# Kernel tuning notes

Hardware: AMD Instinct MI355X
Metric: run time of the kernel (lower is better)

Reference implementation:

```python
import jax, jax.numpy as jnp
import numpy as np

CHEB_K = 2  # chebyshev polynomial order (support_ks = [I, A] for cheb_k=2)


def _fc(x, w1, b1, w2, b2, w3, b3):
    # FC module: Linear -> sigmoid -> Linear -> sigmoid -> Linear
    h = jax.nn.sigmoid(x @ w1 + b1)
    h = jax.nn.sigmoid(h @ w2 + b2)
    return h @ w3 + b3


def _preprocess(adj):
    # adj: [B,N,N]; add self-loops then row-normalize
    adj = adj + jnp.eye(adj.shape[-1], dtype=adj.dtype)
    return adj / adj.sum(-1, keepdims=True)


def _gcn(x, adjs, ne, wpool, bpool):
    # x: [B,N,C], adjs: list of [B,N,N], ne: [N,E]
    # wpool: [E, 2*CHEB_K, C, O], bpool: [E, O]
    mats = []
    for A in adjs:
        ks = [jnp.broadcast_to(jnp.eye(A.shape[-1], dtype=A.dtype), A.shape), A]
        for _ in range(2, CHEB_K):
            ks.append(2.0 * jnp.matmul(A, ks[-1]) - ks[-2])
        mats.extend(ks)
    # [B,N,K,C] with K = 2*CHEB_K
    x_g = jnp.stack([jnp.einsum('bnm,bmc->bnc', S, x) for S in mats], axis=2)
    weights = jnp.einsum('nd,dkio->nkio', ne, wpool)  # [N,K,C,O]
    bias = ne @ bpool  # [N,O]
    return jnp.einsum('bnki,nkio->bno', x_g, weights) + bias


def _forward(x, state, ne0, ne1, ne2, fc1_w1, fc1_b1, fc1_w2, fc1_b2, fc1_w3, fc1_b3,
             fc2_w1, fc2_b1, fc2_w2, fc2_b2, fc2_w3, fc2_b3, gate_w, gate_b, upd_w, upd_b):
    hid = upd_w.shape[-1]
    ins = jnp.concatenate([x, state], axis=-1)  # [B,N,dim_in+hid]
    f1 = _fc(ins, fc1_w1, fc1_b1, fc1_w2, fc1_b2, fc1_w3, fc1_b3)  # [B,N,TD]
    f2 = _fc(ins, fc2_w1, fc2_b1, fc2_w2, fc2_b2, fc2_w3, fc2_b3)
    nv1 = jnp.tanh(ne0[:, None, :] * f1)  # einsum 'bd,bnd->bnd' == broadcast mul
    nv2 = jnp.tanh(ne1[:, None, :] * f2)
    adj = jnp.einsum('bnd,bmd->bnm', nv1, nv2) - jnp.einsum('bnd,bmd->bnm', nv2, nv1)
    adj1 = _preprocess(jax.nn.relu(adj))
    adj2 = _preprocess(jax.nn.relu(-jnp.swapaxes(adj, -2, -1)))
    z_r = jax.nn.sigmoid(_gcn(ins, [adj1, adj2], ne2, gate_w, gate_b))
    z, r = z_r[..., :hid], z_r[..., hid:]
    cand = jnp.concatenate([x, z * state], axis=-1)
    hc = jnp.tanh(_gcn(cand, [adj1, adj2], ne2, upd_w, upd_b))
    return r * state + (1.0 - r) * hc


def setup_inputs():
    B, N, DIN, DOUT, ED, TD = 32, 1024, 2, 64, 10, 32
    HG, MID = 16, 2  # hyperGNN_dim, middle_dim hardcoded in FC
    CIN = DIN + DOUT
    K2 = 2 * CHEB_K
    ks = jax.random.split(jax.random.key(0), 16)
    rn = lambda i, shape, s=1.0: jax.random.normal(ks[i], shape, dtype=jnp.float32) * s
    return {
        'x': rn(0, (B, N, DIN)),
        'state': rn(1, (B, N, DOUT)),
        'ne0': rn(2, (B, TD)),
        'ne1': rn(3, (B, TD)),
        'ne2': rn(4, (N, ED), 0.1),
        'fc1_w1': rn(5, (CIN, HG), 0.1), 'fc1_b1': jnp.zeros((HG,), jnp.float32),
        'fc1_w2': rn(6, (HG, MID), 0.1), 'fc1_b2': jnp.zeros((MID,), jnp.float32),
        'fc1_w3': rn(7, (MID, TD), 0.1), 'fc1_b3': jnp.zeros((TD,), jnp.float32),
        'fc2_w1': rn(8, (CIN, HG), 0.1), 'fc2_b1': jnp.zeros((HG,), jnp.float32),
        'fc2_w2': rn(9, (HG, MID), 0.1), 'fc2_b2': jnp.zeros((MID,), jnp.float32),
        'fc2_w3': rn(10, (MID, TD), 0.1), 'fc2_b3': jnp.zeros((TD,), jnp.float32),
        'gate_w': rn(11, (ED, K2, CIN, 2 * DOUT), 0.1),
        'gate_b': rn(12, (ED, 2 * DOUT), 0.1),
        'upd_w': rn(13, (ED, K2, CIN, DOUT), 0.1),
        'upd_b': rn(14, (ED, DOUT), 0.1),
    }


def reference(x, state, ne0, ne1, ne2, fc1_w1, fc1_b1, fc1_w2, fc1_b2, fc1_w3, fc1_b3,
              fc2_w1, fc2_b1, fc2_w2, fc2_b2, fc2_w3, fc2_b3, gate_w, gate_b, upd_w, upd_b):
    return _forward(x, state, ne0, ne1, ne2, fc1_w1, fc1_b1, fc1_w2, fc1_b2, fc1_w3, fc1_b3,
                    fc2_w1, fc2_b1, fc2_w2, fc2_b2, fc2_w3, fc2_b3, gate_w, gate_b, upd_w, upd_b)
```

## Files before the change

### kernel.cpp

```cpp
#include <hip/hip_runtime.h>
#include <math.h>

#define BB   32
#define NN   1024
#define DIN  2
#define DOUT 64
#define CIN  66
#define TD   32
#define ED   10
#define OG   128
#define OU   64
#define KP   160
#define XTR  80
#define PS   88

typedef __bf16 bf16x8 __attribute__((ext_vector_type(8)));
typedef float  f32x4  __attribute__((ext_vector_type(4)));
typedef short  s16x8  __attribute__((ext_vector_type(8)));

__device__ __forceinline__ unsigned short f2b(float f) {
    __bf16 h = (__bf16)f;
    return *(unsigned short*)&h;
}

__global__ __launch_bounds__(256) void k_pre(
    const float* __restrict__ x, const float* __restrict__ state,
    const float* __restrict__ ne0, const float* __restrict__ ne1,
    const float* __restrict__ ne2,
    const float* __restrict__ w11, const float* __restrict__ b11,
    const float* __restrict__ w12, const float* __restrict__ b12,
    const float* __restrict__ w13, const float* __restrict__ b13,
    const float* __restrict__ w21, const float* __restrict__ b21,
    const float* __restrict__ w22, const float* __restrict__ b22,
    const float* __restrict__ w23, const float* __restrict__ b23,
    const float* __restrict__ gate_w, const float* __restrict__ gate_b,
    const float* __restrict__ upd_w, const float* __restrict__ upd_b,
    unsigned short* __restrict__ nv1b, unsigned short* __restrict__ nv2b,
    unsigned short* __restrict__ XT0, unsigned short* __restrict__ XT1,
    unsigned short* __restrict__ BcTg, unsigned short* __restrict__ BcTu,
    float* __restrict__ biasG, float* __restrict__ biasU)
{
    __shared__ float sw[2408];
    __shared__ unsigned short st[68*72];
    int blk = blockIdx.x;
    int t = threadIdx.x;

    if (blk < 128) {
        const int oW1 = 0, oB1 = 1056, oW2 = 1072, oB2 = 1104, oW3 = 1108, oB3 = 1172, F2 = 1204;
        for (int i = t; i < 1056; i += 256) { sw[oW1+i] = w11[i]; sw[F2+oW1+i] = w21[i]; }
        if (t < 16) { sw[oB1+t] = b11[t]; sw[F2+oB1+t] = b21[t]; }
        if (t < 32) { sw[oW2+t] = w12[t]; sw[F2+oW2+t] = w22[t]; }
        if (t < 2)  { sw[oB2+t] = b12[t]; sw[F2+oB2+t] = b22[t]; }
        if (t < 64) { sw[oW3+t] = w13[t]; sw[F2+oW3+t] = w23[t]; }
        if (t >= 64 && t < 96) { sw[oB3+t-64] = b13[t-64]; sw[F2+oB3+t-64] = b23[t-64]; }
        __syncthreads();

        int p = blk*256 + t;
        int b = p >> 10;

        float h1a[16], h1b[16];
        #pragma unroll
        for (int j = 0; j < 16; ++j) { h1a[j] = sw[oB1+j]; h1b[j] = sw[F2+oB1+j]; }
        for (int i = 0; i < CIN; ++i) {
            float v = (i < DIN) ? x[(size_t)p*DIN + i] : state[(size_t)p*DOUT + (i-DIN)];
            #pragma unroll
            for (int jq = 0; jq < 4; ++jq) {
                float4 wa = *(const float4*)&sw[oW1 + i*16 + jq*4];
                float4 wb = *(const float4*)&sw[F2 + oW1 + i*16 + jq*4];
                h1a[jq*4+0] += v*wa.x; h1a[jq*4+1] += v*wa.y;
                h1a[jq*4+2] += v*wa.z; h1a[jq*4+3] += v*wa.w;
                h1b[jq*4+0] += v*wb.x; h1b[jq*4+1] += v*wb.y;
                h1b[jq*4+2] += v*wb.z; h1b[jq*4+3] += v*wb.w;
            }
        }
        #pragma unroll
        for (int j = 0; j < 16; ++j) {
            h1a[j] = 1.f/(1.f + __expf(-h1a[j]));
            h1b[j] = 1.f/(1.f + __expf(-h1b[j]));
        }
        float h2a0 = sw[oB2+0], h2a1 = sw[oB2+1];
        float h2b0 = sw[F2+oB2+0], h2b1 = sw[F2+oB2+1];
        #pragma unroll
        for (int i = 0; i < 16; ++i) {
            h2a0 += h1a[i]*sw[oW2 + i*2 + 0];
            h2a1 += h1a[i]*sw[oW2 + i*2 + 1];
            h2b0 += h1b[i]*sw[F2+oW2 + i*2 + 0];
            h2b1 += h1b[i]*sw[F2+oW2 + i*2 + 1];
        }
        h2a0 = 1.f/(1.f + __expf(-h2a0)); h2a1 = 1.f/(1.f + __expf(-h2a1));
        h2b0 = 1.f/(1.f + __expf(-h2b0)); h2b1 = 1.f/(1.f + __expf(-h2b1));

        const float* pn0 = ne0 + b*TD;
        const float* pn1 = ne1 + b*TD;
        #pragma unroll
        for (int jq = 0; jq < 8; ++jq) {
            float4 ba  = *(const float4*)&sw[oB3 + jq*4];
            float4 wa0 = *(const float4*)&sw[oW3 + jq*4];
            float4 wa1 = *(const float4*)&sw[oW3 + 32 + jq*4];
            float4 bb2 = *(const float4*)&sw[F2+oB3 + jq*4];
            float4 wb0 = *(const float4*)&sw[F2+oW3 + jq*4];
            float4 wb1 = *(const float4*)&sw[F2+oW3 + 32 + jq*4];
            float4 n0 = *(const float4*)&pn0[jq*4];
            float4 n1 = *(const float4*)&pn1[jq*4];
            ushort4 u1, u2;
            u1.x = f2b(tanhf(n0.x*(ba.x + h2a0*wa0.x + h2a1*wa1.x)));
            u1.y = f2b(tanhf(n0.y*(ba.y + h2a0*wa0.y + h2a1*wa1.y)));
            u1.z = f2b(tanhf(n0.z*(ba.z + h2a0*wa0.z + h2a1*wa1.z)));
            u1.w = f2b(tanhf(n0.w*(ba.w + h2a0*wa0.w + h2a1*wa1.w)));
            u2.x = f2b(tanhf(n1.x*(bb2.x + h2b0*wb0.x + h2b1*wb1.x)));
            u2.y = f2b(tanhf(n1.y*(bb2.y + h2b0*wb0.y + h2b1*wb1.y)));
            u2.z = f2b(tanhf(n1.z*(bb2.z + h2b0*wb0.z + h2b1*wb1.z)));
            u2.w = f2b(tanhf(n1.w*(bb2.w + h2b0*wb0.w + h2b1*wb1.w)));
            *(ushort4*)&nv1b[(size_t)p*TD + jq*4] = u1;
            *(ushort4*)&nv2b[(size_t)p*TD + jq*4] = u2;
        }
    } else if (blk < 640) {
        int idx = blk - 128;
        int b = idx >> 4, m0 = (idx & 15)*64;
        for (int i = t; i < 1024; i += 256) {
            int m = i >> 4, cq = i & 15;
            size_t base = (size_t)b*NN + m0 + m;
            float4 v = *(const float4*)&state[base*DOUT + cq*4];
            st[(2 + cq*4 + 0)*72 + m] = f2b(v.x);
            st[(2 + cq*4 + 1)*72 + m] = f2b(v.y);
            st[(2 + cq*4 + 2)*72 + m] = f2b(v.z);
            st[(2 + cq*4 + 3)*72 + m] = f2b(v.w);
        }
        if (t < 128) {
            int m = t >> 1, c = t & 1;
            st[c*72 + m] = f2b(x[((size_t)b*NN + m0 + m)*DIN + c]);
        }
        __syncthreads();
        const unsigned int ONE2 = 0x3F803F80u;
        for (int i = t; i < XTR*8; i += 256) {
            int c = i >> 3, ch = i & 7;
            uint4 v;
            if (c < 66)      v = *(const uint4*)&st[c*72 + ch*8];
            else if (c == 66) v = make_uint4(ONE2, ONE2, ONE2, ONE2);
            else              v = make_uint4(0, 0, 0, 0);
            *(uint4*)&XT0[((size_t)b*XTR + c)*NN + m0 + ch*8] = v;
            if (c < 2 || c >= 66)
                *(uint4*)&XT1[((size_t)b*XTR + c)*NN + m0 + ch*8] = v;
        }
    } else if (blk < 1840) {
        int tid = (blk - 640)*256 + t;
        int c = tid / KP, k = tid - c*KP;
        const float* pool; int O, cc; unsigned short* dst;
        if (c < 1280) { pool = gate_w; O = OG; cc = c;        dst = BcTg; }
        else          { pool = upd_w;  O = OU; cc = c - 1280; dst = BcTu; }
        int d = cc / O, o = cc - d*O;
        float v = 0.f;
        if (k < 132) {
            int kp = (k < 66) ? 0 : 1;
            int i  = (k < 66) ? k : k - 66;
            v = pool[(size_t)((d*4 + kp)*CIN + i)*O + o]
              + pool[(size_t)((d*4 + kp + 2)*CIN + i)*O + o];
        }
        dst[(size_t)cc*KP + k] = f2b(v);
    } else {
        int i = (blk - 1840)*256 + t;
        int n = i / 192, j = i - n*192;
        float v = 0.f;
        if (j < 128) {
            #pragma unroll
            for (int d = 0; d < ED; ++d) v += ne2[(size_t)n*ED + d]*gate_b[d*OG + j];
            biasG[(size_t)n*OG + j] = v;
        } else {
            int o = j - 128;
            #pragma unroll
            for (int d = 0; d < ED; ++d) v += ne2[(size_t)n*ED + d]*upd_b[d*OU + o];
            biasU[(size_t)n*OU + o] = v;
        }
    }
}

__global__ __launch_bounds__(512) void k_aapply(
    const unsigned short* __restrict__ nv1b, const unsigned short* __restrict__ nv2b,
    const unsigned short* __restrict__ XTg, unsigned short* __restrict__ A)
{
    __shared__ unsigned short s_nv1r[64*40], s_nv2r[64*40];
    __shared__ unsigned short s_nv1c[64*40], s_nv2c[64*40];
    __shared__ unsigned short s_p[64*PS];
    __shared__ unsigned short s_xt[80*72];
    __shared__ float s_rs[64];

    int t = threadIdx.x;
    int id = blockIdx.x;
    int b = id & 31, rbase = (id >> 5)*64;
    int w = t >> 6, lane = t & 63, lq = lane >> 4, ln = lane & 15;
    int g = w >> 1, sub = w & 1;

    {
        int arr = t >> 8, j = t & 255;
        int node = j >> 2, ch = j & 3;
        const unsigned short* src = (arr ? nv2b : nv1b)
            + ((size_t)b*NN + rbase + node)*TD + ch*8;
        unsigned short* dst = (arr ? s_nv2r : s_nv1r) + node*40 + ch*8;
        *(uint4*)dst = *(const uint4*)src;
    }
    __syncthreads();

    bf16x8 a1 = *(const bf16x8*)&s_nv1r[(16*g + ln)*40 + lq*8];
    s16x8 a2s = *(const s16x8*)&s_nv2r[(16*g + ln)*40 + lq*8];
    const s16x8 sgn = {(short)0x8000,(short)0x8000,(short)0x8000,(short)0x8000,
                       (short)0x8000,(short)0x8000,(short)0x8000,(short)0x8000};
    a2s ^= sgn;
    bf16x8 a2n = (bf16x8)a2s;

    f32x4 acc[3];
    #pragma unroll
    for (int i = 0; i < 3; ++i) acc[i] = (f32x4){0.f,0.f,0.f,0.f};
    const f32x4 zero4 = {0.f,0.f,0.f,0.f};

    for (int mb = 0; mb < NN; mb += 64) {
        __syncthreads();
        {
            int arr = t >> 8, j = t & 255;
            int node = j >> 2, ch = j & 3;
            const unsigned short* src = (arr ? nv2b : nv1b)
                + ((size_t)b*NN + mb + node)*TD + ch*8;
            unsigned short* dst = (arr ? s_nv2c : s_nv1c) + node*40 + ch*8;
            *(uint4*)dst = *(const uint4*)src;
        }
        for (int i = t; i < 640; i += 512) {
            int c = i >> 3, ch = i & 7;
            *(uint4*)&s_xt[c*72 + ch*8] =
                *(const uint4*)&XTg[((size_t)b*XTR + c)*NN + mb + ch*8];
        }
        __syncthreads();

        #pragma unroll
        for (int jj = 0; jj < 2; ++jj) {
            int j0 = (sub*2 + jj)*16;
            bf16x8 b2 = *(const bf16x8*)&s_nv2c[(j0 + ln)*40 + lq*8];
            bf16x8 b1 = *(const bf16x8*)&s_nv1c[(j0 + ln)*40 + lq*8];
            f32x4 s = __builtin_amdgcn_mfma_f32_16x16x32_bf16(a1,  b2, zero4, 0, 0, 0);
            s       = __builtin_amdgcn_mfma_f32_16x16x32_bf16(a2n, b1, s,     0, 0, 0);
            #pragma unroll
            for (int r = 0; r < 4; ++r) {
                float p = fmaxf(s[r], 0.f);
                *(__bf16*)&s_p[(16*g + lq*4 + r)*PS + j0 + ln] = (__bf16)p;
            }
        }
        __syncthreads();

        bf16x8 pa0 = *(const bf16x8*)&s_p[(16*g + ln)*PS +      lq*8];
        bf16x8 pa1 = *(const bf16x8*)&s_p[(16*g + ln)*PS + 32 + lq*8];
        if (sub == 0) {
            #pragma unroll
            for (int k = 0; k < 3; ++k) {
                int n0 = k*16;
                bf16x8 xb0 = *(const bf16x8*)&s_xt[(n0 + ln)*72 +      lq*8];
                bf16x8 xb1 = *(const bf16x8*)&s_xt[(n0 + ln)*72 + 32 + lq*8];
                acc[k] = __builtin_amdgcn_mfma_f32_16x16x32_bf16(pa0, xb0, acc[k], 0, 0, 0);
                acc[k] = __builtin_amdgcn_mfma_f32_16x16x32_bf16(pa1, xb1, acc[k], 0, 0, 0);
            }
        } else {
            #pragma unroll
            for (int k = 0; k < 2; ++k) {
                int n0 = (3 + k)*16;
                bf16x8 xb0 = *(const bf16x8*)&s_xt[(n0 + ln)*72 +      lq*8];
                bf16x8 xb1 = *(const bf16x8*)&s_xt[(n0 + ln)*72 + 32 + lq*8];
                acc[k] = __builtin_amdgcn_mfma_f32_16x16x32_bf16(pa0, xb0, acc[k], 0, 0, 0);
                acc[k] = __builtin_amdgcn_mfma_f32_16x16x32_bf16(pa1, xb1, acc[k], 0, 0, 0);
            }
        }
    }

    if (sub == 1 && ln == 2) {
        #pragma unroll
        for (int r = 0; r < 4; ++r) s_rs[16*g + lq*4 + r] = acc[1][r];
    }
    __syncthreads();
    float rinv[4];
    #pragma unroll
    for (int r = 0; r < 4; ++r) rinv[r] = 1.0f / (1.0f + s_rs[16*g + lq*4 + r]);

    int kmax = sub ? 2 : 3;
    for (int k = 0; k < kmax; ++k) {
        int c = (sub ? (3 + k) : k)*16 + ln;
        if (c < CIN) {
            #pragma unroll
            for (int r = 0; r < 4; ++r) {
                int gr = rbase + 16*g + lq*4 + r;
                size_t rowG = (size_t)b*NN + gr;
                unsigned short xu = XTg[((size_t)b*XTR + c)*NN + gr];
                float xr = (float)(*(const __bf16*)&xu);
                A[rowG*KP + c]      = xu;
                A[rowG*KP + 66 + c] = f2b((acc[k][r] + xr) * rinv[r]);
            }
        }
    }
    for (int i = t; i < 64*28; i += 512) {
        int rr = i / 28, cc = 132 + (i - 28*(i/28));
        A[((size_t)b*NN + rbase + rr)*KP + cc] = 0;
    }
}

template<int O, int MODE>
__global__ __launch_bounds__(256) void k_gemm(
    const unsigned short* __restrict__ A, const unsigned short* __restrict__ BcT,
    const float* __restrict__ ne2, const float* __restrict__ biasP,
    const float* __restrict__ state, unsigned short* __restrict__ XT1,
    float* __restrict__ rbuf, float* __restrict__ out)
{
    __shared__ unsigned short s_b[80*168];

    int t = threadIdx.x;
    int w = t >> 6, lane = t & 63, lq = lane >> 4, ln = lane & 15;
    int o0 = blockIdx.y*16;
    int rowBlock = blockIdx.x*128;
    int rowW = rowBlock + w*32;

    f32x4 acc[2][2][5];
    #pragma unroll
    for (int h = 0; h < 2; ++h)
        #pragma unroll
        for (int f = 0; f < 2; ++f)
            #pragma unroll
            for (int c = 0; c < 5; ++c) acc[h][f][c] = (f32x4){0.f,0.f,0.f,0.f};

    #pragma unroll
    for (int h = 0; h < 2; ++h) {
        if (h) __syncthreads();
        for (int i = t; i < 1600; i += 256) {
            int cc = i / 20, kc = i - cc*20;
            int d = h*5 + (cc >> 4), oo = cc & 15;
            *(uint4*)&s_b[cc*168 + kc*8] =
                *(const uint4*)&BcT[(size_t)(d*O + o0 + oo)*KP + kc*8];
        }
        __syncthreads();

        #pragma unroll
        for (int kc = 0; kc < 5; ++kc) {
            bf16x8 af0 = *(const bf16x8*)&A[(size_t)(rowW      + ln)*KP + kc*32 + lq*8];
            bf16x8 af1 = *(const bf16x8*)&A[(size_t)(rowW + 16 + ln)*KP + kc*32 + lq*8];
            #pragma unroll
            for (int ct = 0; ct < 5; ++ct) {
                bf16x8 bf = *(const bf16x8*)&s_b[(ct*16 + ln)*168 + kc*32 + lq*8];
                acc[h][0][ct] = __builtin_amdgcn_mfma_f32_16x16x32_bf16(af0, bf, acc[h][0][ct], 0, 0, 0);
                acc[h][1][ct] = __builtin_amdgcn_mfma_f32_16x16x32_bf16(af1, bf, acc[h][1][ct], 0, 0, 0);
            }
        }
    }

    int o = o0 + ln;
    #pragma unroll
    for (int f = 0; f < 2; ++f) {
        #pragma unroll
        for (int r = 0; r < 4; ++r) {
            int row_l = w*32 + 16*f + lq*4 + r;
            size_t rowG = (size_t)rowBlock + row_l;
            int n = (int)(rowG & (NN - 1));
            int bb = (int)(rowG >> 10);
            const float* nep = &ne2[(size_t)n*ED];
            float val = biasP[(size_t)n*O + o];
            #pragma unroll
            for (int d = 0; d < 5; ++d) val += nep[d]     * acc[0][f][d][r];
            #pragma unroll
            for (int d = 0; d < 5; ++d) val += nep[5 + d] * acc[1][f][d][r];
            if (MODE == 0) {
                float sv = 1.f/(1.f + __expf(-val));
                if (o0 < 64) {
                    float zst = sv * state[rowG*DOUT + o];
                    XT1[((size_t)bb*XTR + 2 + o)*NN + n] = f2b(zst);
                } else {
                    rbuf[rowG*DOUT + (o - 64)] = sv;
                }
            } else {
                float hc = tanhf(val);
                float rg = rbuf[rowG*DOUT + o];
                float st = state[rowG*DOUT + o];
                out[rowG*DOUT + o] = rg*st + (1.f - rg)*hc;
            }
        }
    }
}

extern "C" void kernel_launch(void* const* d_in, const int* in_sizes, int n_in,
                              void* d_out, int out_size, void* d_ws, size_t ws_size,
                              hipStream_t stream)
{
    const float* x      = (const float*)d_in[0];
    const float* state  = (const float*)d_in[1];
    const float* ne0    = (const float*)d_in[2];
    const float* ne1    = (const float*)d_in[3];
    const float* ne2    = (const float*)d_in[4];
    const float* f1w1   = (const float*)d_in[5];
    const float* f1b1   = (const float*)d_in[6];
    const float* f1w2   = (const float*)d_in[7];
    const float* f1b2   = (const float*)d_in[8];
    const float* f1w3   = (const float*)d_in[9];
    const float* f1b3   = (const float*)d_in[10];
    const float* f2w1   = (const float*)d_in[11];
    const float* f2b1   = (const float*)d_in[12];
    const float* f2w2   = (const float*)d_in[13];
    const float* f2b2   = (const float*)d_in[14];
    const float* f2w3   = (const float*)d_in[15];
    const float* f2b3   = (const float*)d_in[16];
    const float* gate_w = (const float*)d_in[17];
    const float* gate_b = (const float*)d_in[18];
    const float* upd_w  = (const float*)d_in[19];
    const float* upd_b  = (const float*)d_in[20];

    unsigned short* nv1b = (unsigned short*)d_ws;
    unsigned short* nv2b = nv1b + (size_t)BB*NN*TD;
    unsigned short* XT0  = nv2b + (size_t)BB*NN*TD;
    unsigned short* XT1  = XT0  + (size_t)BB*XTR*NN;
    unsigned short* A    = XT1  + (size_t)BB*XTR*NN;
    unsigned short* BcTg = A    + (size_t)BB*NN*KP;
    unsigned short* BcTu = BcTg + (size_t)1280*KP;
    float* biasG = (float*)(BcTu + (size_t)640*KP);
    float* biasU = biasG + (size_t)NN*OG;
    float* rbuf  = biasU + (size_t)NN*OU;
    float* out   = (float*)d_out;

    k_pre<<<dim3(2608), 256, 0, stream>>>(x, state, ne0, ne1, ne2,
        f1w1, f1b1, f1w2, f1b2, f1w3, f1b3,
        f2w1, f2b1, f2w2, f2b2, f2w3, f2b3,
        gate_w, gate_b, upd_w, upd_b,
        nv1b, nv2b, XT0, XT1, BcTg, BcTu, biasG, biasU);

    k_aapply<<<dim3(512), 512, 0, stream>>>(nv1b, nv2b, XT0, A);

    k_gemm<OG,0><<<dim3(BB*NN/128, 8), 256, 0, stream>>>(A, BcTg, ne2, biasG,
                                                         state, XT1, rbuf, nullptr);

    k_aapply<<<dim3(512), 512, 0, stream>>>(nv1b, nv2b, XT1, A);

    k_gemm<OU,1><<<dim3(BB*NN/128, 4), 256, 0, stream>>>(A, BcTu, ne2, biasU,
                                                         state, nullptr, rbuf, out);
}
```

Measured before the change: 235.7 us.

## Fuse adjacency-apply and weight GEMM into one kernel via shared memory

```diff
diff --git a/kernel.cpp b/kernel.cpp
--- a/kernel.cpp
+++ b/kernel.cpp
@@ -13,6 +13,7 @@
 #define KP   160
 #define XTR  80
 #define PS   88
+#define SAS  168
 
 typedef __bf16 bf16x8 __attribute__((ext_vector_type(8)));
 typedef float  f32x4  __attribute__((ext_vector_type(4)));
@@ -174,15 +175,27 @@
     }
 }
 
-__global__ __launch_bounds__(512) void k_aapply(
+template<int O, int MODE>
+__global__ __launch_bounds__(512) void k_fused(
     const unsigned short* __restrict__ nv1b, const unsigned short* __restrict__ nv2b,
-    const unsigned short* __restrict__ XTg, unsigned short* __restrict__ A)
+    const unsigned short* __restrict__ XTg, const unsigned short* __restrict__ BcT,
+    const float* __restrict__ ne2, const float* __restrict__ biasP,
+    const float* __restrict__ state, unsigned short* __restrict__ XT1,
+    float* __restrict__ rbuf, float* __restrict__ out)
 {
-    __shared__ unsigned short s_nv1r[64*40], s_nv2r[64*40];
-    __shared__ unsigned short s_nv1c[64*40], s_nv2c[64*40];
-    __shared__ unsigned short s_p[64*PS];
-    __shared__ unsigned short s_xt[80*72];
-    __shared__ float s_rs[64];
+    union SM {
+        struct {
+            unsigned short nv1r[64*40], nv2r[64*40], nv1c[64*40], nv2c[64*40];
+            unsigned short p[64*PS];
+            unsigned short xt[80*72];
+            float rs[64];
+        } aa;
+        struct {
+            unsigned short a[64*SAS];
+            unsigned short bb[4][32*SAS];
+        } ge;
+    };
+    __shared__ SM sm;
 
     int t = threadIdx.x;
     int id = blockIdx.x;
@@ -195,13 +208,13 @@
         int node = j >> 2, ch = j & 3;
         const unsigned short* src = (arr ? nv2b : nv1b)
             + ((size_t)b*NN + rbase + node)*TD + ch*8;
-        unsigned short* dst = (arr ? s_nv2r : s_nv1r) + node*40 + ch*8;
+        unsigned short* dst = (arr ? sm.aa.nv2r : sm.aa.nv1r) + node*40 + ch*8;
         *(uint4*)dst = *(const uint4*)src;
     }
     __syncthreads();
 
-    bf16x8 a1 = *(const bf16x8*)&s_nv1r[(16*g + ln)*40 + lq*8];
-    s16x8 a2s = *(const s16x8*)&s_nv2r[(16*g + ln)*40 + lq*8];
+    bf16x8 a1 = *(const bf16x8*)&sm.aa.nv1r[(16*g + ln)*40 + lq*8];
+    s16x8 a2s = *(const s16x8*)&sm.aa.nv2r[(16*g + ln)*40 + lq*8];
     const s16x8 sgn = {(short)0x8000,(short)0x8000,(short)0x8000,(short)0x8000,
                        (short)0x8000,(short)0x8000,(short)0x8000,(short)0x8000};
     a2s ^= sgn;
@@ -219,12 +232,12 @@
             int node = j >> 2, ch = j & 3;
             const unsigned short* src = (arr ? nv2b : nv1b)
                 + ((size_t)b*NN + mb + node)*TD + ch*8;
-            unsigned short* dst = (arr ? s_nv2c : s_nv1c) + node*40 + ch*8;
+            unsigned short* dst = (arr ? sm.aa.nv2c : sm.aa.nv1c) + node*40 + ch*8;
             *(uint4*)dst = *(const uint4*)src;
         }
         for (int i = t; i < 640; i += 512) {
             int c = i >> 3, ch = i & 7;
-            *(uint4*)&s_xt[c*72 + ch*8] =
+            *(uint4*)&sm.aa.xt[c*72 + ch*8] =
                 *(const uint4*)&XTg[((size_t)b*XTR + c)*NN + mb + ch*8];
         }
         __syncthreads();
@@ -232,26 +245,26 @@
         #pragma unroll
         for (int jj = 0; jj < 2; ++jj) {
             int j0 = (sub*2 + jj)*16;
-            bf16x8 b2 = *(const bf16x8*)&s_nv2c[(j0 + ln)*40 + lq*8];
-            bf16x8 b1 = *(const bf16x8*)&s_nv1c[(j0 + ln)*40 + lq*8];
+            bf16x8 b2 = *(const bf16x8*)&sm.aa.nv2c[(j0 + ln)*40 + lq*8];
+            bf16x8 b1 = *(const bf16x8*)&sm.aa.nv1c[(j0 + ln)*40 + lq*8];
             f32x4 s = __builtin_amdgcn_mfma_f32_16x16x32_bf16(a1,  b2, zero4, 0, 0, 0);
             s       = __builtin_amdgcn_mfma_f32_16x16x32_bf16(a2n, b1, s,     0, 0, 0);
             #pragma unroll
             for (int r = 0; r < 4; ++r) {
                 float p = fmaxf(s[r], 0.f);
-                *(__bf16*)&s_p[(16*g + lq*4 + r)*PS + j0 + ln] = (__bf16)p;
+                *(__bf16*)&sm.aa.p[(16*g + lq*4 + r)*PS + j0 + ln] = (__bf16)p;
             }
         }
         __syncthreads();
 
-        bf16x8 pa0 = *(const bf16x8*)&s_p[(16*g + ln)*PS +      lq*8];
-        bf16x8 pa1 = *(const bf16x8*)&s_p[(16*g + ln)*PS + 32 + lq*8];
+        bf16x8 pa0 = *(const bf16x8*)&sm.aa.p[(16*g + ln)*PS +      lq*8];
+        bf16x8 pa1 = *(const bf16x8*)&sm.aa.p[(16*g + ln)*PS + 32 + lq*8];
         if (sub == 0) {
             #pragma unroll
             for (int k = 0; k < 3; ++k) {
                 int n0 = k*16;
-                bf16x8 xb0 = *(const bf16x8*)&s_xt[(n0 + ln)*72 +      lq*8];
-                bf16x8 xb1 = *(const bf16x8*)&s_xt[(n0 + ln)*72 + 32 + lq*8];
+                bf16x8 xb0 = *(const bf16x8*)&sm.aa.xt[(n0 + ln)*72 +      lq*8];
+                bf16x8 xb1 = *(const bf16x8*)&sm.aa.xt[(n0 + ln)*72 + 32 + lq*8];
                 acc[k] = __builtin_amdgcn_mfma_f32_16x16x32_bf16(pa0, xb0, acc[k], 0, 0, 0);
                 acc[k] = __builtin_amdgcn_mfma_f32_16x16x32_bf16(pa1, xb1, acc[k], 0, 0, 0);
             }
@@ -259,8 +272,8 @@
             #pragma unroll
             for (int k = 0; k < 2; ++k) {
                 int n0 = (3 + k)*16;
-                bf16x8 xb0 = *(const bf16x8*)&s_xt[(n0 + ln)*72 +      lq*8];
-                bf16x8 xb1 = *(const bf16x8*)&s_xt[(n0 + ln)*72 + 32 + lq*8];
+                bf16x8 xb0 = *(const bf16x8*)&sm.aa.xt[(n0 + ln)*72 +      lq*8];
+                bf16x8 xb1 = *(const bf16x8*)&sm.aa.xt[(n0 + ln)*72 + 32 + lq*8];
                 acc[k] = __builtin_amdgcn_mfma_f32_16x16x32_bf16(pa0, xb0, acc[k], 0, 0, 0);
                 acc[k] = __builtin_amdgcn_mfma_f32_16x16x32_bf16(pa1, xb1, acc[k], 0, 0, 0);
             }
@@ -269,109 +282,103 @@
 
     if (sub == 1 && ln == 2) {
         #pragma unroll
-        for (int r = 0; r < 4; ++r) s_rs[16*g + lq*4 + r] = acc[1][r];
+        for (int r = 0; r < 4; ++r) sm.aa.rs[16*g + lq*4 + r] = acc[1][r];
     }
     __syncthreads();
     float rinv[4];
     #pragma unroll
-    for (int r = 0; r < 4; ++r) rinv[r] = 1.0f / (1.0f + s_rs[16*g + lq*4 + r]);
-
-    int kmax = sub ? 2 : 3;
-    for (int k = 0; k < kmax; ++k) {
-        int c = (sub ? (3 + k) : k)*16 + ln;
-        if (c < CIN) {
+    for (int r = 0; r < 4; ++r) rinv[r] = 1.0f / (1.0f + sm.aa.rs[16*g + lq*4 + r]);
+    __syncthreads();
+
+    {
+        int kmax = sub ? 2 : 3;
+        for (int k = 0; k < kmax; ++k) {
+            int c = (sub ? (3 + k) : k)*16 + ln;
+            if (c < CIN) {
+                #pragma unroll
+                for (int r = 0; r < 4; ++r) {
+                    int row_l = 16*g + lq*4 + r;
+                    int gr = rbase + row_l;
+                    unsigned short xu = XTg[((size_t)b*XTR + c)*NN + gr];
+                    float xr = (float)(*(const __bf16*)&xu);
+                    sm.ge.a[row_l*SAS + c]      = xu;
+                    sm.ge.a[row_l*SAS + 66 + c] = f2b((acc[k][r] + xr) * rinv[r]);
+                }
+            }
+        }
+        for (int i = t; i < 64*36; i += 512) {
+            int row = i / 36, cc = 132 + (i - 36*(i/36));
+            sm.ge.a[row*SAS + cc] = 0;
+        }
+    }
+
+    const int rg = w >> 2;
+    const int sl = w & 3;
+    const int ITERS = O/16/4;
+
+    for (int iter = 0; iter < ITERS; ++iter) {
+        int o0 = (iter*4 + sl)*16;
+        int o = o0 + ln;
+
+        f32x4 gacc[ED][2];
+        #pragma unroll
+        for (int d = 0; d < ED; ++d) {
+            gacc[d][0] = (f32x4){0.f,0.f,0.f,0.f};
+            gacc[d][1] = (f32x4){0.f,0.f,0.f,0.f};
+        }
+
+        for (int chunk = 0; chunk < 5; ++chunk) {
+            __syncthreads();
+            for (int i = t; i < 2560; i += 512) {
+                int isl = i / 640, rem = i - isl*640;
+                int cc = rem / 20, kc = rem - cc*20;
+                int d = chunk*2 + (cc >> 4), oo = cc & 15;
+                int o0s = (iter*4 + isl)*16;
+                *(uint4*)&sm.ge.bb[isl][cc*SAS + kc*8] =
+                    *(const uint4*)&BcT[(size_t)(d*O + o0s + oo)*KP + kc*8];
+            }
+            __syncthreads();
+
+            #pragma unroll
+            for (int kc = 0; kc < 5; ++kc) {
+                bf16x8 af0 = *(const bf16x8*)&sm.ge.a[(rg*32      + ln)*SAS + kc*32 + lq*8];
+                bf16x8 af1 = *(const bf16x8*)&sm.ge.a[(rg*32 + 16 + ln)*SAS + kc*32 + lq*8];
+                #pragma unroll
+                for (int ctl = 0; ctl < 2; ++ctl) {
+                    int d = chunk*2 + ctl;
+                    bf16x8 bf = *(const bf16x8*)&sm.ge.bb[sl][(ctl*16 + ln)*SAS + kc*32 + lq*8];
+                    gacc[d][0] = __builtin_amdgcn_mfma_f32_16x16x32_bf16(af0, bf, gacc[d][0], 0, 0, 0);
+                    gacc[d][1] = __builtin_amdgcn_mfma_f32_16x16x32_bf16(af1, bf, gacc[d][1], 0, 0, 0);
+                }
+            }
+        }
+
+        #pragma unroll
+        for (int f = 0; f < 2; ++f) {
             #pragma unroll
             for (int r = 0; r < 4; ++r) {
-                int gr = rbase + 16*g + lq*4 + r;
-                size_t rowG = (size_t)b*NN + gr;
-                unsigned short xu = XTg[((size_t)b*XTR + c)*NN + gr];
-                float xr = (float)(*(const __bf16*)&xu);
-                A[rowG*KP + c]      = xu;
-                A[rowG*KP + 66 + c] = f2b((acc[k][r] + xr) * rinv[r]);
-            }
-        }
-    }
-    for (int i = t; i < 64*28; i += 512) {
-        int rr = i / 28, cc = 132 + (i - 28*(i/28));
-        A[((size_t)b*NN + rbase + rr)*KP + cc] = 0;
-    }
-}
-
-template<int O, int MODE>
-__global__ __launch_bounds__(256) void k_gemm(
-    const unsigned short* __restrict__ A, const unsigned short* __restrict__ BcT,
-    const float* __restrict__ ne2, const float* __restrict__ biasP,
-    const float* __restrict__ state, unsigned short* __restrict__ XT1,
-    float* __restrict__ rbuf, float* __restrict__ out)
-{
-    __shared__ unsigned short s_b[80*168];
-
-    int t = threadIdx.x;
-    int w = t >> 6, lane = t & 63, lq = lane >> 4, ln = lane & 15;
-    int o0 = blockIdx.y*16;
-    int rowBlock = blockIdx.x*128;
-    int rowW = rowBlock + w*32;
-
-    f32x4 acc[2][2][5];
-    #pragma unroll
-    for (int h = 0; h < 2; ++h)
-        #pragma unroll
-        for (int f = 0; f < 2; ++f)
-            #pragma unroll
-            for (int c = 0; c < 5; ++c) acc[h][f][c] = (f32x4){0.f,0.f,0.f,0.f};
-
-    #pragma unroll
-    for (int h = 0; h < 2; ++h) {
-        if (h) __syncthreads();
-        for (int i = t; i < 1600; i += 256) {
-            int cc = i / 20, kc = i - cc*20;
-            int d = h*5 + (cc >> 4), oo = cc & 15;
-            *(uint4*)&s_b[cc*168 + kc*8] =
-                *(const uint4*)&BcT[(size_t)(d*O + o0 + oo)*KP + kc*8];
-        }
-        __syncthreads();
-
-        #pragma unroll
-        for (int kc = 0; kc < 5; ++kc) {
-            bf16x8 af0 = *(const bf16x8*)&A[(size_t)(rowW      + ln)*KP + kc*32 + lq*8];
-            bf16x8 af1 = *(const bf16x8*)&A[(size_t)(rowW + 16 + ln)*KP + kc*32 + lq*8];
-            #pragma unroll
-            for (int ct = 0; ct < 5; ++ct) {
-                bf16x8 bf = *(const bf16x8*)&s_b[(ct*16 + ln)*168 + kc*32 + lq*8];
-                acc[h][0][ct] = __builtin_amdgcn_mfma_f32_16x16x32_bf16(af0, bf, acc[h][0][ct], 0, 0, 0);
-                acc[h][1][ct] = __builtin_amdgcn_mfma_f32_16x16x32_bf16(af1, bf, acc[h][1][ct], 0, 0, 0);
-            }
-        }
-    }
-
-    int o = o0 + ln;
-    #pragma unroll
-    for (int f = 0; f < 2; ++f) {
-        #pragma unroll
-        for (int r = 0; r < 4; ++r) {
-            int row_l = w*32 + 16*f + lq*4 + r;
-            size_t rowG = (size_t)rowBlock + row_l;
-            int n = (int)(rowG & (NN - 1));
-            int bb = (int)(rowG >> 10);
-            const float* nep = &ne2[(size_t)n*ED];
-            float val = biasP[(size_t)n*O + o];
-            #pragma unroll
-            for (int d = 0; d < 5; ++d) val += nep[d]     * acc[0][f][d][r];
-            #pragma unroll
-            for (int d = 0; d < 5; ++d) val += nep[5 + d] * acc[1][f][d][r];
-            if (MODE == 0) {
-                float sv = 1.f/(1.f + __expf(-val));
-                if (o0 < 64) {
-                    float zst = sv * state[rowG*DOUT + o];
-                    XT1[((size_t)bb*XTR + 2 + o)*NN + n] = f2b(zst);
+                int row_l = rg*32 + 16*f + lq*4 + r;
+                int n = rbase + row_l;
+                size_t rowG = (size_t)b*NN + n;
+                const float* nep = &ne2[(size_t)n*ED];
+                float val = biasP[(size_t)n*O + o];
+                #pragma unroll
+                for (int d = 0; d < ED; ++d)
+                    val += nep[d] * gacc[d][f][r];
+                if (MODE == 0) {
+                    float sv = 1.f/(1.f + __expf(-val));
+                    if (o0 < 64) {
+                        float zst = sv * state[rowG*DOUT + o];
+                        XT1[((size_t)b*XTR + 2 + o)*NN + n] = f2b(zst);
+                    } else {
+                        rbuf[rowG*DOUT + (o - 64)] = sv;
+                    }
                 } else {
-                    rbuf[rowG*DOUT + (o - 64)] = sv;
+                    float hc = tanhf(val);
+                    float rg2 = rbuf[rowG*DOUT + o];
+                    float st = state[rowG*DOUT + o];
+                    out[rowG*DOUT + o] = rg2*st + (1.f - rg2)*hc;
                 }
-            } else {
-                float hc = tanhf(val);
-                float rg = rbuf[rowG*DOUT + o];
-                float st = state[rowG*DOUT + o];
-                out[rowG*DOUT + o] = rg*st + (1.f - rg)*hc;
             }
         }
     }
@@ -407,8 +414,7 @@
     unsigned short* nv2b = nv1b + (size_t)BB*NN*TD;
     unsigned short* XT0  = nv2b + (size_t)BB*NN*TD;
     unsigned short* XT1  = XT0  + (size_t)BB*XTR*NN;
-    unsigned short* A    = XT1  + (size_t)BB*XTR*NN;
-    unsigned short* BcTg = A    + (size_t)BB*NN*KP;
+    unsigned short* BcTg = XT1  + (size_t)BB*XTR*NN;
     unsigned short* BcTu = BcTg + (size_t)1280*KP;
     float* biasG = (float*)(BcTu + (size_t)640*KP);
     float* biasU = biasG + (size_t)NN*OG;
@@ -421,13 +427,9 @@
         gate_w, gate_b, upd_w, upd_b,
         nv1b, nv2b, XT0, XT1, BcTg, BcTu, biasG, biasU);
 
-    k_aapply<<<dim3(512), 512, 0, stream>>>(nv1b, nv2b, XT0, A);
-
-    k_gemm<OG,0><<<dim3(BB*NN/128, 8), 256, 0, stream>>>(A, BcTg, ne2, biasG,
-                                                         state, XT1, rbuf, nullptr);
-
-    k_aapply<<<dim3(512), 512, 0, stream>>>(nv1b, nv2b, XT1, A);
-
-    k_gemm<OU,1><<<dim3(BB*NN/128, 4), 256, 0, stream>>>(A, BcTu, ne2, biasU,
-                                                         state, nullptr, rbuf, out);
+    k_fused<OG,0><<<dim3(512), 512, 0, stream>>>(nv1b, nv2b, XT0, BcTg,
+        ne2, biasG, state, XT1, rbuf, nullptr);
+
+    k_fused<OU,1><<<dim3(512), 512, 0, stream>>>(nv1b, nv2b, XT1, BcTu,
+        ne2, biasU, state, nullptr, rbuf, out);
 }
```

Measured after the change: 376.7 us. 1.6x slower.

## Double-buffer nv and XT tiles in k_aapply and remap prep-kernel indexing

Applied to the files above, without the earlier changes.

```diff
diff --git a/kernel.cpp b/kernel.cpp
--- a/kernel.cpp
+++ b/kernel.cpp
@@ -144,7 +144,7 @@
         }
     } else if (blk < 1840) {
         int tid = (blk - 640)*256 + t;
-        int c = tid / KP, k = tid - c*KP;
+        int k = tid / 1920, c = tid - k*1920;
         const float* pool; int O, cc; unsigned short* dst;
         if (c < 1280) { pool = gate_w; O = OG; cc = c;        dst = BcTg; }
         else          { pool = upd_w;  O = OU; cc = c - 1280; dst = BcTu; }
@@ -179,9 +179,9 @@
     const unsigned short* __restrict__ XTg, unsigned short* __restrict__ A)
 {
     __shared__ unsigned short s_nv1r[64*40], s_nv2r[64*40];
-    __shared__ unsigned short s_nv1c[64*40], s_nv2c[64*40];
+    __shared__ unsigned short s_nv1c[2][64*40], s_nv2c[2][64*40];
     __shared__ unsigned short s_p[64*PS];
-    __shared__ unsigned short s_xt[80*72];
+    __shared__ unsigned short s_xt[2][80*72];
     __shared__ float s_rs[64];
 
     int t = threadIdx.x;
@@ -198,6 +198,19 @@
         unsigned short* dst = (arr ? s_nv2r : s_nv1r) + node*40 + ch*8;
         *(uint4*)dst = *(const uint4*)src;
     }
+    {
+        int arr = t >> 8, j = t & 255;
+        int node = j >> 2, ch = j & 3;
+        const unsigned short* src = (arr ? nv2b : nv1b)
+            + ((size_t)b*NN + node)*TD + ch*8;
+        unsigned short* dst = (arr ? s_nv2c[0] : s_nv1c[0]) + node*40 + ch*8;
+        *(uint4*)dst = *(const uint4*)src;
+    }
+    for (int i = t; i < 640; i += 512) {
+        int c = i >> 3, ch = i & 7;
+        *(uint4*)&s_xt[0][c*72 + ch*8] =
+            *(const uint4*)&XTg[((size_t)b*XTR + c)*NN + ch*8];
+    }
     __syncthreads();
 
     bf16x8 a1 = *(const bf16x8*)&s_nv1r[(16*g + ln)*40 + lq*8];
@@ -212,28 +225,14 @@
     for (int i = 0; i < 3; ++i) acc[i] = (f32x4){0.f,0.f,0.f,0.f};
     const f32x4 zero4 = {0.f,0.f,0.f,0.f};
 
-    for (int mb = 0; mb < NN; mb += 64) {
-        __syncthreads();
-        {
-            int arr = t >> 8, j = t & 255;
-            int node = j >> 2, ch = j & 3;
-            const unsigned short* src = (arr ? nv2b : nv1b)
-                + ((size_t)b*NN + mb + node)*TD + ch*8;
-            unsigned short* dst = (arr ? s_nv2c : s_nv1c) + node*40 + ch*8;
-            *(uint4*)dst = *(const uint4*)src;
-        }
-        for (int i = t; i < 640; i += 512) {
-            int c = i >> 3, ch = i & 7;
-            *(uint4*)&s_xt[c*72 + ch*8] =
-                *(const uint4*)&XTg[((size_t)b*XTR + c)*NN + mb + ch*8];
-        }
-        __syncthreads();
+    for (int it = 0; it < 16; ++it) {
+        int buf = it & 1;
 
         #pragma unroll
         for (int jj = 0; jj < 2; ++jj) {
             int j0 = (sub*2 + jj)*16;
-            bf16x8 b2 = *(const bf16x8*)&s_nv2c[(j0 + ln)*40 + lq*8];
-            bf16x8 b1 = *(const bf16x8*)&s_nv1c[(j0 + ln)*40 + lq*8];
+            bf16x8 b2 = *(const bf16x8*)&s_nv2c[buf][(j0 + ln)*40 + lq*8];
+            bf16x8 b1 = *(const bf16x8*)&s_nv1c[buf][(j0 + ln)*40 + lq*8];
             f32x4 s = __builtin_amdgcn_mfma_f32_16x16x32_bf16(a1,  b2, zero4, 0, 0, 0);
             s       = __builtin_amdgcn_mfma_f32_16x16x32_bf16(a2n, b1, s,     0, 0, 0);
             #pragma unroll
@@ -250,8 +249,8 @@
             #pragma unroll
             for (int k = 0; k < 3; ++k) {
                 int n0 = k*16;
-                bf16x8 xb0 = *(const bf16x8*)&s_xt[(n0 + ln)*72 +      lq*8];
-                bf16x8 xb1 = *(const bf16x8*)&s_xt[(n0 + ln)*72 + 32 + lq*8];
+                bf16x8 xb0 = *(const bf16x8*)&s_xt[buf][(n0 + ln)*72 +      lq*8];
+                bf16x8 xb1 = *(const bf16x8*)&s_xt[buf][(n0 + ln)*72 + 32 + lq*8];
                 acc[k] = __builtin_amdgcn_mfma_f32_16x16x32_bf16(pa0, xb0, acc[k], 0, 0, 0);
                 acc[k] = __builtin_amdgcn_mfma_f32_16x16x32_bf16(pa1, xb1, acc[k], 0, 0, 0);
             }
@@ -259,12 +258,31 @@
             #pragma unroll
             for (int k = 0; k < 2; ++k) {
                 int n0 = (3 + k)*16;
-                bf16x8 xb0 = *(const bf16x8*)&s_xt[(n0 + ln)*72 +      lq*8];
-                bf16x8 xb1 = *(const bf16x8*)&s_xt[(n0 + ln)*72 + 32 + lq*8];
+                bf16x8 xb0 = *(const bf16x8*)&s_xt[buf][(n0 + ln)*72 +      lq*8];
+                bf16x8 xb1 = *(const bf16x8*)&s_xt[buf][(n0 + ln)*72 + 32 + lq*8];
                 acc[k] = __builtin_amdgcn_mfma_f32_16x16x32_bf16(pa0, xb0, acc[k], 0, 0, 0);
                 acc[k] = __builtin_amdgcn_mfma_f32_16x16x32_bf16(pa1, xb1, acc[k], 0, 0, 0);
             }
         }
+
+        if (it < 15) {
+            int mbn = (it + 1)*64;
+            int nbuf = buf ^ 1;
+            {
+                int arr = t >> 8, j = t & 255;
+                int node = j >> 2, ch = j & 3;
+                const unsigned short* src = (arr ? nv2b : nv1b)
+                    + ((size_t)b*NN + mbn + node)*TD + ch*8;
+                unsigned short* dst = (arr ? s_nv2c[nbuf] : s_nv1c[nbuf]) + node*40 + ch*8;
+                *(uint4*)dst = *(const uint4*)src;
+            }
+            for (int i = t; i < 640; i += 512) {
+                int c = i >> 3, ch = i & 7;
+                *(uint4*)&s_xt[nbuf][c*72 + ch*8] =
+                    *(const uint4*)&XTg[((size_t)b*XTR + c)*NN + mbn + ch*8];
+            }
+        }
+        __syncthreads();
     }
 
     if (sub == 1 && ln == 2) {
```

Result: no change. 236.6 us (+0.4%).
